# Optimization experiments

Measured on AMD Instinct MI355X. Metric: run time of the kernel, lower is better.

The kernel has to match this reference:

```python
import jax, jax.numpy as jnp
import numpy as np

K, A, DIM = 1024, 16384, 512


def setup_inputs() -> dict:
    key = jax.random.key(0)
    ks = jax.random.split(key, 8)
    B, H, W = 2048, 8, 8
    z_t = jax.random.randint(ks[0], (B, H, W), 0, K, dtype=jnp.int64)
    z_tp1 = jax.random.randint(ks[1], (B, H, W), 0, K, dtype=jnp.int64)
    embed_w = jax.random.normal(ks[2], (K, DIM), dtype=jnp.float32) * 0.02
    # MLP: Linear(2*dim -> dim), GELU, Linear(dim -> dim)
    lim1 = 1.0 / np.sqrt(2 * DIM)
    w1 = jax.random.uniform(ks[3], (2 * DIM, DIM), minval=-lim1, maxval=lim1, dtype=jnp.float32)
    b1 = jax.random.uniform(ks[4], (DIM,), minval=-lim1, maxval=lim1, dtype=jnp.float32)
    lim2 = 1.0 / np.sqrt(DIM)
    w2 = jax.random.uniform(ks[5], (DIM, DIM), minval=-lim2, maxval=lim2, dtype=jnp.float32)
    b2 = jax.random.uniform(ks[6], (DIM,), minval=-lim2, maxval=lim2, dtype=jnp.float32)
    codebook_w = jax.random.normal(ks[7], (A, DIM), dtype=jnp.float32) * 0.02
    return {"z_t": z_t, "z_tp1": z_tp1, "embed_w": embed_w, "w1": w1, "b1": b1,
            "w2": w2, "b2": b2, "codebook_w": codebook_w}


def reference(z_t, z_tp1, embed_w, w1, b1, w2, b2, codebook_w):
    B = z_t.shape[0]
    # embed int code grids and mean-pool over H*W tokens -> [B, dim]
    e_t = embed_w[z_t.reshape(B, -1)].mean(axis=1)
    e_tp1 = embed_w[z_tp1.reshape(B, -1)].mean(axis=1)
    h = jnp.concatenate([e_t, e_tp1], axis=-1)          # [B, 2*dim]
    h = jax.nn.gelu(h @ w1 + b1, approximate=False)
    e = h @ w2 + b2                                      # [B, dim]
    # VQ: squared L2 distance to each code, argmin, gather
    d2 = (jnp.sum(e * e, axis=1, keepdims=True)
          - 2.0 * e @ codebook_w.T
          + jnp.sum(codebook_w * codebook_w, axis=1)[None, :])  # [B, A]
    ids = jnp.argmin(d2, axis=1)                         # [B]
    q = codebook_w[ids]                                  # [B, dim]
    return ids, q
```

## Files before the change

### kernel.cpp

```cpp
#include <hip/hip_runtime.h>
#include <hip/hip_bf16.h>

#define TOK 64
#define DIMC 512

typedef __attribute__((ext_vector_type(8))) short v8s;
typedef __attribute__((ext_vector_type(4))) float v4f;

__device__ __forceinline__ unsigned int f2ord(float f) {
  unsigned int u = __float_as_uint(f);
  return (u & 0x80000000u) ? ~u : (u | 0x80000000u);
}

__device__ __forceinline__ float gelu_exact(float x) {
  return 0.5f * x * (1.0f + erff(x * 0.70710678118654752440f));
}

__device__ __forceinline__ unsigned short f2bf(float x) {
  unsigned int u = __float_as_uint(x);
  return (unsigned short)((u + 0x7FFFu + ((u >> 16) & 1u)) >> 16);
}
__device__ __forceinline__ float bf2f(unsigned short h) {
  return __uint_as_float((unsigned int)h << 16);
}

__device__ __forceinline__ void gl2lds16(const void* g, void* l) {
  __builtin_amdgcn_global_load_lds((const __attribute__((address_space(1))) void*)g,
                                   (__attribute__((address_space(3))) void*)l,
                                   16, 0, 0);
}

__global__ __launch_bounds__(256) void k_prep(
    const int* __restrict__ zt, const int* __restrict__ ztp,
    const float* __restrict__ emb,
    unsigned short* __restrict__ hh, unsigned short* __restrict__ hl,
    unsigned long long* __restrict__ rowmin,
    const float* __restrict__ w1, unsigned short* __restrict__ w1th,
    unsigned short* __restrict__ w1tl,
    const float* __restrict__ w2, unsigned short* __restrict__ w2th,
    unsigned short* __restrict__ w2tl,
    const float* __restrict__ cb, unsigned short* __restrict__ ch,
    unsigned short* __restrict__ cl, float* __restrict__ cnorm) {
  __shared__ int codes[128];
  __shared__ float tbuf[32][33];
  const int bid = blockIdx.x;
  const int tid = threadIdx.x;

  if (bid < 2048) {
    const int b = bid;
    if (tid < 64) codes[tid] = zt[b * TOK + tid];
    else if (tid < 128) codes[tid] = ztp[b * TOK + (tid - 64)];
    if (tid == 0) rowmin[b] = 0xFFFFFFFFFFFFFFFFull;
    __syncthreads();
    const int half = tid >> 7;
    const int c4 = tid & 127;
    const float4* emb4 = (const float4*)emb;
    float4 s = make_float4(0.f, 0.f, 0.f, 0.f);
    #pragma unroll 8
    for (int t = 0; t < TOK; t++) {
      const int code = codes[half * TOK + t];
      const float4 v = emb4[code * 128 + c4];
      s.x += v.x; s.y += v.y; s.z += v.z; s.w += v.w;
    }
    const float inv = 1.0f / 64.0f;
    float f[4] = {s.x * inv, s.y * inv, s.z * inv, s.w * inv};
    unsigned short hi[4], lo[4];
    #pragma unroll
    for (int i = 0; i < 4; i++) {
      hi[i] = f2bf(f[i]);
      lo[i] = f2bf(f[i] - bf2f(hi[i]));
    }
    const int off = b * 1024 + half * 512 + c4 * 4;
    *(ushort4*)&hh[off] = make_ushort4(hi[0], hi[1], hi[2], hi[3]);
    *(ushort4*)&hl[off] = make_ushort4(lo[0], lo[1], lo[2], lo[3]);
  } else if (bid < 2816) {
    const float* w; unsigned short *wth, *wtl; int Kd, N, k0, n0;
    if (bid < 2560) {
      const int i = bid - 2048;
      w = w1; wth = w1th; wtl = w1tl; Kd = 1024; N = 512;
      k0 = (i & 31) * 32; n0 = (i >> 5) * 32;
    } else {
      const int i = bid - 2560;
      w = w2; wth = w2th; wtl = w2tl; Kd = 512; N = 512;
      k0 = (i & 15) * 32; n0 = (i >> 4) * 32;
    }
    const int c = tid & 31, r = tid >> 5;
    #pragma unroll
    for (int i = 0; i < 4; i++)
      tbuf[r + i * 8][c] = w[(size_t)(k0 + r + i * 8) * N + n0 + c];
    __syncthreads();
    #pragma unroll
    for (int i = 0; i < 4; i++) {
      const float v = tbuf[c][r + i * 8];
      const unsigned short hi = f2bf(v);
      const unsigned short lo = f2bf(v - bf2f(hi));
      wth[(size_t)(n0 + r + i * 8) * Kd + k0 + c] = hi;
      wtl[(size_t)(n0 + r + i * 8) * Kd + k0 + c] = lo;
    }
  } else {
    const int row = (bid - 2816) * 4 + (tid >> 6);
    const int lane = tid & 63;
    const float4* cb4 = (const float4*)cb;
    const float4 va = cb4[row * 128 + lane * 2];
    const float4 vb = cb4[row * 128 + lane * 2 + 1];
    float s = va.x * va.x + va.y * va.y + va.z * va.z + va.w * va.w
            + vb.x * vb.x + vb.y * vb.y + vb.z * vb.z + vb.w * vb.w;
    float f[8] = {va.x, va.y, va.z, va.w, vb.x, vb.y, vb.z, vb.w};
    unsigned short hi[8], lo[8];
    #pragma unroll
    for (int i = 0; i < 8; i++) {
      hi[i] = f2bf(f[i]);
      lo[i] = f2bf(f[i] - bf2f(hi[i]));
    }
    ushort4* chp = (ushort4*)&ch[row * DIMC + lane * 8];
    ushort4* clp = (ushort4*)&cl[row * DIMC + lane * 8];
    chp[0] = make_ushort4(hi[0], hi[1], hi[2], hi[3]);
    chp[1] = make_ushort4(hi[4], hi[5], hi[6], hi[7]);
    clp[0] = make_ushort4(lo[0], lo[1], lo[2], lo[3]);
    clp[1] = make_ushort4(lo[4], lo[5], lo[6], lo[7]);
    #pragma unroll
    for (int off = 32; off > 0; off >>= 1) s += __shfl_down(s, off);
    if (lane == 0) cnorm[row] = s;
  }
}

template <bool GELU>
__global__ __launch_bounds__(256) void k_gemm(const unsigned short* __restrict__ Ah_,
                                              const unsigned short* __restrict__ Al_,
                                              const unsigned short* __restrict__ Bh_,
                                              const unsigned short* __restrict__ Bl_,
                                              const float* __restrict__ bias,
                                              unsigned short* __restrict__ oh,
                                              unsigned short* __restrict__ ol,
                                              int Kd, int N) {
  __shared__ unsigned short AhS[2][32 * 32];
  __shared__ unsigned short AlS[2][32 * 32];
  __shared__ unsigned short BhS[2][64 * 32];
  __shared__ unsigned short BlS[2][64 * 32];

  const int tid = threadIdx.x;
  const int lane = tid & 63;
  const int wid = tid >> 6;
  const int m0 = blockIdx.x * 32;
  const int n0 = blockIdx.y * 64;

  const unsigned short* Ab_h = Ah_ + (size_t)m0 * Kd;
  const unsigned short* Ab_l = Al_ + (size_t)m0 * Kd;
  const unsigned short* Bb_h = Bh_ + (size_t)n0 * Kd;
  const unsigned short* Bb_l = Bl_ + (size_t)n0 * Kd;

  const int srow = lane >> 2;
  const int sk = (lane & 3) * 8;
  const int wm = wid >> 1, wn = wid & 1;
  const int fr = lane & 15;
  const int fq = (lane >> 4) * 8;

  v4f acc[2];
  acc[0] = (v4f)(0.f);
  acc[1] = (v4f)(0.f);

  auto stage = [&](int b, int k0) {
    #pragma unroll
    for (int u = 0; u < 3; u++) {
      const int i = wid * 3 + u;
      const unsigned short* gs; unsigned short* ls; int rbase;
      if (i < 2)      { gs = Ab_h; ls = AhS[b]; rbase = i * 16; }
      else if (i < 4) { gs = Ab_l; ls = AlS[b]; rbase = (i - 2) * 16; }
      else if (i < 8) { gs = Bb_h; ls = BhS[b]; rbase = (i - 4) * 16; }
      else            { gs = Bb_l; ls = BlS[b]; rbase = (i - 8) * 16; }
      gl2lds16(gs + (size_t)(rbase + srow) * Kd + k0 + sk, ls + rbase * 32);
    }
  };

  stage(0, 0);
  int cur = 0;
  for (int k0 = 0; k0 < Kd; k0 += 32) {
    __syncthreads();
    if (k0 + 32 < Kd) stage(cur ^ 1, k0 + 32);

    const int ar = (wm * 16 + fr) * 32 + fq;
    const v8s ah = *(const v8s*)&AhS[cur][ar];
    const v8s al = *(const v8s*)&AlS[cur][ar];
    #pragma unroll
    for (int nt = 0; nt < 2; nt++) {
      const int br = (wn * 32 + nt * 16 + fr) * 32 + fq;
      const v8s bh = *(const v8s*)&BhS[cur][br];
      const v8s bl = *(const v8s*)&BlS[cur][br];
      acc[nt] = __builtin_amdgcn_mfma_f32_16x16x32_bf16(ah, bh, acc[nt], 0, 0, 0);
      acc[nt] = __builtin_amdgcn_mfma_f32_16x16x32_bf16(ah, bl, acc[nt], 0, 0, 0);
      acc[nt] = __builtin_amdgcn_mfma_f32_16x16x32_bf16(al, bh, acc[nt], 0, 0, 0);
    }
    cur ^= 1;
  }

  const int col16 = lane & 15;
  const int q = lane >> 4;
  #pragma unroll
  for (int nt = 0; nt < 2; nt++) {
    const int col = n0 + wn * 32 + nt * 16 + col16;
    const float bv = bias[col];
    #pragma unroll
    for (int reg = 0; reg < 4; reg++) {
      const int row = m0 + wm * 16 + q * 4 + reg;
      float v = acc[nt][reg] + bv;
      if (GELU) v = gelu_exact(v);
      const unsigned short hi = f2bf(v);
      oh[(size_t)row * N + col] = hi;
      ol[(size_t)row * N + col] = f2bf(v - bf2f(hi));
    }
  }
}

__global__ __launch_bounds__(256, 2) void k_vq(const unsigned short* __restrict__ eh,
                                               const unsigned short* __restrict__ el,
                                               const unsigned short* __restrict__ ch,
                                               const unsigned short* __restrict__ cl,
                                               const float* __restrict__ cnorm,
                                               unsigned long long* __restrict__ rowmin) {
  __shared__ unsigned short Ah[128 * 32];
  __shared__ unsigned short Al[128 * 32];
  __shared__ unsigned short Bh[256 * 32];
  __shared__ unsigned short Bl[256 * 32];

  const int tid = threadIdx.x;
  const int lane = tid & 63;
  const int wid = tid >> 6;
  const int bid = blockIdx.x;
  const int j = bid >> 3;
  const int x = j & 15;
  const int y = ((j >> 4) << 3) | (bid & 7);
  const int r0 = x * 128;
  const int c0 = y * 256;

  v4f acc[4][8];
  #pragma unroll
  for (int i = 0; i < 4; i++)
    #pragma unroll
    for (int jj = 0; jj < 8; jj++) acc[i][jj] = (v4f)(0.f);

  const unsigned short* ehB = eh + (size_t)r0 * DIMC;
  const unsigned short* elB = el + (size_t)r0 * DIMC;
  const unsigned short* chB = ch + (size_t)c0 * DIMC;
  const unsigned short* clB = cl + (size_t)c0 * DIMC;

  const int srow = lane >> 2;
  const int sk = (lane & 3) * 8;
  const int wm = wid >> 1;
  const int wn = wid & 1;
  const int fr = lane & 15;
  const int fq = (lane >> 4) * 8;

  for (int k0 = 0; k0 < DIMC; k0 += 32) {
    __syncthreads();
    #pragma unroll
    for (int u = 0; u < 12; u++) {
      const int i = wid * 12 + u;
      const unsigned short* gs; unsigned short* ls; int rbase;
      if (i < 8)       { gs = ehB; ls = Ah; rbase = i * 16; }
      else if (i < 16) { gs = elB; ls = Al; rbase = (i - 8) * 16; }
      else if (i < 32) { gs = chB; ls = Bh; rbase = (i - 16) * 16; }
      else             { gs = clB; ls = Bl; rbase = (i - 32) * 16; }
      gl2lds16(gs + (size_t)(rbase + srow) * DIMC + k0 + sk, ls + rbase * 32);
    }
    __syncthreads();

    v8s ahf[4], alf[4];
    #pragma unroll
    for (int mt = 0; mt < 4; mt++) {
      const int ar = (wm * 64 + mt * 16 + fr) * 32 + fq;
      ahf[mt] = *(const v8s*)&Ah[ar];
      alf[mt] = *(const v8s*)&Al[ar];
    }
    #pragma unroll
    for (int nt = 0; nt < 8; nt++) {
      const int br = (wn * 128 + nt * 16 + fr) * 32 + fq;
      const v8s bhf = *(const v8s*)&Bh[br];
      const v8s blf = *(const v8s*)&Bl[br];
      #pragma unroll
      for (int mt = 0; mt < 4; mt++) {
        acc[mt][nt] = __builtin_amdgcn_mfma_f32_16x16x32_bf16(ahf[mt], bhf, acc[mt][nt], 0, 0, 0);
        acc[mt][nt] = __builtin_amdgcn_mfma_f32_16x16x32_bf16(ahf[mt], blf, acc[mt][nt], 0, 0, 0);
        acc[mt][nt] = __builtin_amdgcn_mfma_f32_16x16x32_bf16(alf[mt], bhf, acc[mt][nt], 0, 0, 0);
      }
    }
  }

  const int col16 = lane & 15;
  const int q = lane >> 4;
  float cn[8];
  #pragma unroll
  for (int nt = 0; nt < 8; nt++) cn[nt] = cnorm[c0 + wn * 128 + nt * 16 + col16];

  #pragma unroll
  for (int mt = 0; mt < 4; mt++) {
    #pragma unroll
    for (int reg = 0; reg < 4; reg++) {
      const int row = r0 + wm * 64 + mt * 16 + q * 4 + reg;
      float best = fmaf(-2.f, acc[mt][0][reg], cn[0]);
      int bid2 = c0 + wn * 128 + col16;
      #pragma unroll
      for (int nt = 1; nt < 8; nt++) {
        const float s = fmaf(-2.f, acc[mt][nt][reg], cn[nt]);
        const int id = c0 + wn * 128 + nt * 16 + col16;
        if (s < best) { best = s; bid2 = id; }
      }
      unsigned long long v =
          ((unsigned long long)f2ord(best) << 32) | (unsigned int)bid2;
      #pragma unroll
      for (int off = 8; off > 0; off >>= 1) {
        const unsigned long long o = __shfl_down(v, off, 16);
        if (o < v) v = o;
      }
      if (col16 == 0) atomicMin(&rowmin[row], v);
    }
  }
}

__global__ __launch_bounds__(64) void k_final(const unsigned long long* __restrict__ rowmin,
                                              const float* __restrict__ cb,
                                              float* __restrict__ out,
                                              int B) {
  const int b = blockIdx.x;
  const int t = threadIdx.x;
  const unsigned long long m = rowmin[b];
  const int id = (int)(unsigned int)(m & 0xFFFFFFFFull);
  if (t == 0) out[b] = (float)id;
  float4* q4 = (float4*)(out + B) + b * 128;
  const float4* cb4 = (const float4*)cb + (size_t)id * 128;
  q4[t] = cb4[t];
  q4[t + 64] = cb4[t + 64];
}

extern "C" void kernel_launch(void* const* d_in, const int* in_sizes, int n_in,
                              void* d_out, int out_size, void* d_ws, size_t ws_size,
                              hipStream_t stream) {
  const int* zt = (const int*)d_in[0];
  const int* ztp = (const int*)d_in[1];
  const float* emb = (const float*)d_in[2];
  const float* w1 = (const float*)d_in[3];
  const float* b1 = (const float*)d_in[4];
  const float* w2 = (const float*)d_in[5];
  const float* b2 = (const float*)d_in[6];
  const float* cb = (const float*)d_in[7];
  float* out = (float*)d_out;

  const int B = in_sizes[0] / TOK;
  const int A = in_sizes[7] / DIMC;

  char* p = (char*)d_ws;
  unsigned short* hh = (unsigned short*)p;  p += (size_t)B * 1024 * 2;
  unsigned short* hl = (unsigned short*)p;  p += (size_t)B * 1024 * 2;
  unsigned short* w1th = (unsigned short*)p; p += (size_t)512 * 1024 * 2;
  unsigned short* w1tl = (unsigned short*)p; p += (size_t)512 * 1024 * 2;
  unsigned short* w2th = (unsigned short*)p; p += (size_t)512 * 512 * 2;
  unsigned short* w2tl = (unsigned short*)p; p += (size_t)512 * 512 * 2;
  unsigned short* h1h = (unsigned short*)p; p += (size_t)B * DIMC * 2;
  unsigned short* h1l = (unsigned short*)p; p += (size_t)B * DIMC * 2;
  unsigned short* eh = (unsigned short*)p;  p += (size_t)B * DIMC * 2;
  unsigned short* el = (unsigned short*)p;  p += (size_t)B * DIMC * 2;
  unsigned short* ch = (unsigned short*)p;  p += (size_t)A * DIMC * 2;
  unsigned short* cl = (unsigned short*)p;  p += (size_t)A * DIMC * 2;
  float* cnorm = (float*)p;                 p += (size_t)A * 4;
  unsigned long long* rowmin = (unsigned long long*)p;

  k_prep<<<2816 + A / 4, 256, 0, stream>>>(zt, ztp, emb, hh, hl, rowmin,
                                           w1, w1th, w1tl, w2, w2th, w2tl,
                                           cb, ch, cl, cnorm);
  k_gemm<true><<<dim3(B / 32, 512 / 64), 256, 0, stream>>>(hh, hl, w1th, w1tl, b1, h1h, h1l, 1024, 512);
  k_gemm<false><<<dim3(B / 32, 512 / 64), 256, 0, stream>>>(h1h, h1l, w2th, w2tl, b2, eh, el, 512, 512);
  k_vq<<<(B / 128) * (A / 256), 256, 0, stream>>>(eh, el, ch, cl, cnorm, rowmin);
  k_final<<<B, 64, 0, stream>>>(rowmin, cb, out, B);
}
```

Before: 229.1 us.

## Triple-buffer VQ GEMM loads with swizzled LDS and 512-thread blocks

Restructures the VQ distance GEMM kernel to use a three-stage LDS ring buffer, issuing global-to-LDS loads two k-steps ahead and waiting with partial vmcnt counts instead of full syncs. The LDS layout gets an XOR swizzle to cut bank conflicts on fragment reads. Blocks grow to 512 threads with 8 waves each covering a 64x64 subtile, which halves accumulator registers per wave. s_setprio is raised around the MFMA section. The cost is more LDS per block (about 144KB), which may limit occupancy to one block per CU.

```diff
diff --git a/kernel.cpp b/kernel.cpp
--- a/kernel.cpp
+++ b/kernel.cpp
@@ -211,16 +211,18 @@
   }
 }
 
-__global__ __launch_bounds__(256, 2) void k_vq(const unsigned short* __restrict__ eh,
+__device__ __forceinline__ const v8s* fragp(const unsigned short* base, int row, int slot) {
+  const int byte = ((row << 6) | (slot << 4)) ^ ((row & 7) << 4);
+  return (const v8s*)((const char*)base + byte);
+}
+
+__global__ __launch_bounds__(512, 2) void k_vq(const unsigned short* __restrict__ eh,
                                                const unsigned short* __restrict__ el,
                                                const unsigned short* __restrict__ ch,
                                                const unsigned short* __restrict__ cl,
                                                const float* __restrict__ cnorm,
                                                unsigned long long* __restrict__ rowmin) {
-  __shared__ unsigned short Ah[128 * 32];
-  __shared__ unsigned short Al[128 * 32];
-  __shared__ unsigned short Bh[256 * 32];
-  __shared__ unsigned short Bl[256 * 32];
+  __shared__ unsigned short lds[3 * 24576];
 
   const int tid = threadIdx.x;
   const int lane = tid & 63;
@@ -232,64 +234,91 @@
   const int r0 = x * 128;
   const int c0 = y * 256;
 
-  v4f acc[4][8];
-  #pragma unroll
-  for (int i = 0; i < 4; i++)
-    #pragma unroll
-    for (int jj = 0; jj < 8; jj++) acc[i][jj] = (v4f)(0.f);
-
   const unsigned short* ehB = eh + (size_t)r0 * DIMC;
   const unsigned short* elB = el + (size_t)r0 * DIMC;
   const unsigned short* chB = ch + (size_t)c0 * DIMC;
   const unsigned short* clB = cl + (size_t)c0 * DIMC;
 
-  const int srow = lane >> 2;
-  const int sk = (lane & 3) * 8;
-  const int wm = wid >> 1;
-  const int wn = wid & 1;
+  const int L0 = lane & 1, L1 = (lane >> 1) & 1, L2 = (lane >> 2) & 1;
+  const int L3 = (lane >> 3) & 1, L4 = (lane >> 4) & 1, L5 = (lane >> 5) & 1;
+  const int lrow = (L2 ^ L4) | (L3 << 1) | (L4 << 2) | (L5 << 3);
+  const int lcol = ((L0 ^ L2 ^ L4) | ((L1 ^ L3) << 1)) * 8;
+
+  const int wm = wid >> 2;
+  const int wn = wid & 3;
   const int fr = lane & 15;
-  const int fq = (lane >> 4) * 8;
-
-  for (int k0 = 0; k0 < DIMC; k0 += 32) {
-    __syncthreads();
-    #pragma unroll
-    for (int u = 0; u < 12; u++) {
-      const int i = wid * 12 + u;
-      const unsigned short* gs; unsigned short* ls; int rbase;
-      if (i < 8)       { gs = ehB; ls = Ah; rbase = i * 16; }
-      else if (i < 16) { gs = elB; ls = Al; rbase = (i - 8) * 16; }
-      else if (i < 32) { gs = chB; ls = Bh; rbase = (i - 16) * 16; }
-      else             { gs = clB; ls = Bl; rbase = (i - 32) * 16; }
-      gl2lds16(gs + (size_t)(rbase + srow) * DIMC + k0 + sk, ls + rbase * 32);
-    }
-    __syncthreads();
-
-    v8s ahf[4], alf[4];
+  const int q = lane >> 4;
+
+  v4f acc[4][4];
+  #pragma unroll
+  for (int i = 0; i < 4; i++)
+    #pragma unroll
+    for (int jj = 0; jj < 4; jj++) acc[i][jj] = (v4f)(0.f);
+
+  const unsigned short* gp[6];
+  int lo[6];
+  #pragma unroll
+  for (int u = 0; u < 6; u++) {
+    const int i = wid * 6 + u;
+    const unsigned short* gs; int off, rbase;
+    if (i < 8)       { gs = ehB; off = 0;     rbase = i * 16; }
+    else if (i < 16) { gs = elB; off = 4096;  rbase = (i - 8) * 16; }
+    else if (i < 32) { gs = chB; off = 8192;  rbase = (i - 16) * 16; }
+    else             { gs = clB; off = 16384; rbase = (i - 32) * 16; }
+    gp[u] = gs + (size_t)(rbase + lrow) * DIMC + lcol;
+    lo[u] = off + rbase * 32;
+  }
+
+  auto stage = [&](int buf, int k0) {
+    #pragma unroll
+    for (int u = 0; u < 6; u++)
+      gl2lds16(gp[u] + k0, lds + buf * 24576 + lo[u]);
+  };
+
+  stage(0, 0);
+  stage(1, 32);
+  asm volatile("s_waitcnt vmcnt(6)" ::: "memory");
+  __builtin_amdgcn_s_barrier();
+
+  #pragma unroll
+  for (int t = 0; t < 16; ++t) {
+    const int cb_ = t % 3;
+    if (t < 14) stage((t + 2) % 3, (t + 2) * 32);
+
+    const unsigned short* base = lds + cb_ * 24576;
+    v8s ah[4], al[4];
     #pragma unroll
     for (int mt = 0; mt < 4; mt++) {
-      const int ar = (wm * 64 + mt * 16 + fr) * 32 + fq;
-      ahf[mt] = *(const v8s*)&Ah[ar];
-      alf[mt] = *(const v8s*)&Al[ar];
-    }
-    #pragma unroll
-    for (int nt = 0; nt < 8; nt++) {
-      const int br = (wn * 128 + nt * 16 + fr) * 32 + fq;
-      const v8s bhf = *(const v8s*)&Bh[br];
-      const v8s blf = *(const v8s*)&Bl[br];
+      const int ar = wm * 64 + mt * 16 + fr;
+      ah[mt] = *fragp(base, ar, q);
+      al[mt] = *fragp(base + 4096, ar, q);
+    }
+    __builtin_amdgcn_s_setprio(1);
+    #pragma unroll
+    for (int nt = 0; nt < 4; nt++) {
+      const int br = wn * 64 + nt * 16 + fr;
+      const v8s bh = *fragp(base + 8192, br, q);
+      const v8s bl = *fragp(base + 16384, br, q);
       #pragma unroll
       for (int mt = 0; mt < 4; mt++) {
-        acc[mt][nt] = __builtin_amdgcn_mfma_f32_16x16x32_bf16(ahf[mt], bhf, acc[mt][nt], 0, 0, 0);
-        acc[mt][nt] = __builtin_amdgcn_mfma_f32_16x16x32_bf16(ahf[mt], blf, acc[mt][nt], 0, 0, 0);
-        acc[mt][nt] = __builtin_amdgcn_mfma_f32_16x16x32_bf16(alf[mt], bhf, acc[mt][nt], 0, 0, 0);
+        acc[mt][nt] = __builtin_amdgcn_mfma_f32_16x16x32_bf16(ah[mt], bh, acc[mt][nt], 0, 0, 0);
+        acc[mt][nt] = __builtin_amdgcn_mfma_f32_16x16x32_bf16(ah[mt], bl, acc[mt][nt], 0, 0, 0);
+        acc[mt][nt] = __builtin_amdgcn_mfma_f32_16x16x32_bf16(al[mt], bh, acc[mt][nt], 0, 0, 0);
       }
     }
+    __builtin_amdgcn_s_setprio(0);
+
+    if (t < 15) {
+      if (t < 14) asm volatile("s_waitcnt vmcnt(6)" ::: "memory");
+      else        asm volatile("s_waitcnt vmcnt(0)" ::: "memory");
+      __builtin_amdgcn_s_barrier();
+    }
   }
 
   const int col16 = lane & 15;
-  const int q = lane >> 4;
-  float cn[8];
-  #pragma unroll
-  for (int nt = 0; nt < 8; nt++) cn[nt] = cnorm[c0 + wn * 128 + nt * 16 + col16];
+  float cn[4];
+  #pragma unroll
+  for (int nt = 0; nt < 4; nt++) cn[nt] = cnorm[c0 + wn * 64 + nt * 16 + col16];
 
   #pragma unroll
   for (int mt = 0; mt < 4; mt++) {
@@ -297,11 +326,11 @@
     for (int reg = 0; reg < 4; reg++) {
       const int row = r0 + wm * 64 + mt * 16 + q * 4 + reg;
       float best = fmaf(-2.f, acc[mt][0][reg], cn[0]);
-      int bid2 = c0 + wn * 128 + col16;
+      int bid2 = c0 + wn * 64 + col16;
       #pragma unroll
-      for (int nt = 1; nt < 8; nt++) {
+      for (int nt = 1; nt < 4; nt++) {
         const float s = fmaf(-2.f, acc[mt][nt][reg], cn[nt]);
-        const int id = c0 + wn * 128 + nt * 16 + col16;
+        const int id = c0 + wn * 64 + nt * 16 + col16;
         if (s < best) { best = s; bid2 = id; }
       }
       unsigned long long v =
@@ -368,6 +397,6 @@
                                            cb, ch, cl, cnorm);
   k_gemm<true><<<dim3(B / 32, 512 / 64), 256, 0, stream>>>(hh, hl, w1th, w1tl, b1, h1h, h1l, 1024, 512);
   k_gemm<false><<<dim3(B / 32, 512 / 64), 256, 0, stream>>>(h1h, h1l, w2th, w2tl, b2, eh, el, 512, 512);
-  k_vq<<<(B / 128) * (A / 256), 256, 0, stream>>>(eh, el, ch, cl, cnorm, rowmin);
+  k_vq<<<(B / 128) * (A / 256), 512, 0, stream>>>(eh, el, ch, cl, cnorm, rowmin);
   k_final<<<B, 64, 0, stream>>>(rowmin, cb, out, B);
 }
```

After: 247.3 us. 7.9% more time.

## Double-buffer VQ LDS tiles and enlarge block to 256x256 with 8 waves

Applied to the files above, without the earlier changes.

The VQ distance GEMM now uses 512-thread blocks covering 256 rows by 256 codes, with a single double-buffered LDS array. The next K-slice is prefetched while MFMAs run on the current one, removing one barrier per iteration. Wave priority is raised around the MFMA section. The aim is to hide global-to-LDS latency and halve codebook reloads. In exchange, LDS use grows to 128KB per block, which limits occupancy and may conflict with the launch bound of 2 blocks.

```diff
diff --git a/kernel.cpp b/kernel.cpp
--- a/kernel.cpp
+++ b/kernel.cpp
@@ -211,32 +211,22 @@
   }
 }
 
-__global__ __launch_bounds__(256, 2) void k_vq(const unsigned short* __restrict__ eh,
+__global__ __launch_bounds__(512, 2) void k_vq(const unsigned short* __restrict__ eh,
                                                const unsigned short* __restrict__ el,
                                                const unsigned short* __restrict__ ch,
                                                const unsigned short* __restrict__ cl,
                                                const float* __restrict__ cnorm,
                                                unsigned long long* __restrict__ rowmin) {
-  __shared__ unsigned short Ah[128 * 32];
-  __shared__ unsigned short Al[128 * 32];
-  __shared__ unsigned short Bh[256 * 32];
-  __shared__ unsigned short Bl[256 * 32];
+  __shared__ unsigned short lds[2 * 32768];
 
   const int tid = threadIdx.x;
   const int lane = tid & 63;
   const int wid = tid >> 6;
   const int bid = blockIdx.x;
-  const int j = bid >> 3;
-  const int x = j & 15;
-  const int y = ((j >> 4) << 3) | (bid & 7);
-  const int r0 = x * 128;
+  const int x = (bid >> 3) & 7;
+  const int y = (((bid >> 6) & 7) << 3) | (bid & 7);
+  const int r0 = x * 256;
   const int c0 = y * 256;
-
-  v4f acc[4][8];
-  #pragma unroll
-  for (int i = 0; i < 4; i++)
-    #pragma unroll
-    for (int jj = 0; jj < 8; jj++) acc[i][jj] = (v4f)(0.f);
 
   const unsigned short* ehB = eh + (size_t)r0 * DIMC;
   const unsigned short* elB = el + (size_t)r0 * DIMC;
@@ -248,45 +238,67 @@
   const int wm = wid >> 1;
   const int wn = wid & 1;
   const int fr = lane & 15;
-  const int fq = (lane >> 4) * 8;
-
-  for (int k0 = 0; k0 < DIMC; k0 += 32) {
-    __syncthreads();
-    #pragma unroll
-    for (int u = 0; u < 12; u++) {
-      const int i = wid * 12 + u;
-      const unsigned short* gs; unsigned short* ls; int rbase;
-      if (i < 8)       { gs = ehB; ls = Ah; rbase = i * 16; }
-      else if (i < 16) { gs = elB; ls = Al; rbase = (i - 8) * 16; }
-      else if (i < 32) { gs = chB; ls = Bh; rbase = (i - 16) * 16; }
-      else             { gs = clB; ls = Bl; rbase = (i - 32) * 16; }
-      gl2lds16(gs + (size_t)(rbase + srow) * DIMC + k0 + sk, ls + rbase * 32);
-    }
-    __syncthreads();
-
-    v8s ahf[4], alf[4];
+  const int q = lane >> 4;
+  const int fq = q * 8;
+
+  v4f acc[4][8];
+  #pragma unroll
+  for (int i = 0; i < 4; i++)
+    #pragma unroll
+    for (int jj = 0; jj < 8; jj++) acc[i][jj] = (v4f)(0.f);
+
+  const unsigned short* gp[8];
+  int lo_[8];
+  #pragma unroll
+  for (int u = 0; u < 8; u++) {
+    const int i = wid * 8 + u;
+    const unsigned short* gs; int off, rbase;
+    if (i < 16)      { gs = ehB; off = 0;     rbase = i * 16; }
+    else if (i < 32) { gs = elB; off = 8192;  rbase = (i - 16) * 16; }
+    else if (i < 48) { gs = chB; off = 16384; rbase = (i - 32) * 16; }
+    else             { gs = clB; off = 24576; rbase = (i - 48) * 16; }
+    gp[u] = gs + (size_t)(rbase + srow) * DIMC + sk;
+    lo_[u] = off + rbase * 32;
+  }
+
+  auto stage = [&](int buf, int k0) {
+    #pragma unroll
+    for (int u = 0; u < 8; u++)
+      gl2lds16(gp[u] + k0, lds + buf * 32768 + lo_[u]);
+  };
+
+  stage(0, 0);
+  __syncthreads();
+
+  for (int t = 0; t < 16; ++t) {
+    if (t < 15) stage((t + 1) & 1, (t + 1) * 32);
+
+    const unsigned short* base = lds + (t & 1) * 32768;
+    v8s ah[4], al[4];
     #pragma unroll
     for (int mt = 0; mt < 4; mt++) {
       const int ar = (wm * 64 + mt * 16 + fr) * 32 + fq;
-      ahf[mt] = *(const v8s*)&Ah[ar];
-      alf[mt] = *(const v8s*)&Al[ar];
-    }
+      ah[mt] = *(const v8s*)&base[ar];
+      al[mt] = *(const v8s*)&base[8192 + ar];
+    }
+    __builtin_amdgcn_s_setprio(1);
     #pragma unroll
     for (int nt = 0; nt < 8; nt++) {
       const int br = (wn * 128 + nt * 16 + fr) * 32 + fq;
-      const v8s bhf = *(const v8s*)&Bh[br];
-      const v8s blf = *(const v8s*)&Bl[br];
+      const v8s bh = *(const v8s*)&base[16384 + br];
+      const v8s bl = *(const v8s*)&base[24576 + br];
       #pragma unroll
       for (int mt = 0; mt < 4; mt++) {
-        acc[mt][nt] = __builtin_amdgcn_mfma_f32_16x16x32_bf16(ahf[mt], bhf, acc[mt][nt], 0, 0, 0);
-        acc[mt][nt] = __builtin_amdgcn_mfma_f32_16x16x32_bf16(ahf[mt], blf, acc[mt][nt], 0, 0, 0);
-        acc[mt][nt] = __builtin_amdgcn_mfma_f32_16x16x32_bf16(alf[mt], bhf, acc[mt][nt], 0, 0, 0);
+        acc[mt][nt] = __builtin_amdgcn_mfma_f32_16x16x32_bf16(ah[mt], bh, acc[mt][nt], 0, 0, 0);
+        acc[mt][nt] = __builtin_amdgcn_mfma_f32_16x16x32_bf16(ah[mt], bl, acc[mt][nt], 0, 0, 0);
+        acc[mt][nt] = __builtin_amdgcn_mfma_f32_16x16x32_bf16(al[mt], bh, acc[mt][nt], 0, 0, 0);
       }
     }
+    __builtin_amdgcn_s_setprio(0);
+    if (t < 15) __syncthreads();
   }
 
   const int col16 = lane & 15;
-  const int q = lane >> 4;
   float cn[8];
   #pragma unroll
   for (int nt = 0; nt < 8; nt++) cn[nt] = cnorm[c0 + wn * 128 + nt * 16 + col16];
@@ -368,6 +380,6 @@
                                            cb, ch, cl, cnorm);
   k_gemm<true><<<dim3(B / 32, 512 / 64), 256, 0, stream>>>(hh, hl, w1th, w1tl, b1, h1h, h1l, 1024, 512);
   k_gemm<false><<<dim3(B / 32, 512 / 64), 256, 0, stream>>>(h1h, h1l, w2th, w2tl, b2, eh, el, 512, 512);
-  k_vq<<<(B / 128) * (A / 256), 256, 0, stream>>>(eh, el, ch, cl, cnorm, rowmin);
+  k_vq<<<(B / 256) * (A / 256), 512, 0, stream>>>(eh, el, ch, cl, cnorm, rowmin);
   k_final<<<B, 64, 0, stream>>>(rowmin, cb, out, B);
 }
```

Result: faster. 224.2 us (-2.1%).
